# Kernel optimization log

Hardware: AMD Instinct MI355X
Metric: run time of the kernel (lower is better)

Reference implementation:

```python
import jax, jax.numpy as jnp
import numpy as np
import math

B, T, F, H, A = 32, 2048, 2048, 1024, 512


def setup_inputs() -> dict:
    key = jax.random.key(0)
    ks = jax.random.split(key, 8)
    def xavier(k, shape):
        fan_out, fan_in = shape
        bound = math.sqrt(6.0 / (fan_in + fan_out))
        return jax.random.uniform(k, shape, jnp.float32, -bound, bound)
    return {
        "features": jax.random.normal(ks[0], (B, T, F), jnp.float32),
        "hidden": jax.random.normal(ks[1], (B, H), jnp.float32),
        "W_h": xavier(ks[2], (A, H)),
        "b_h": jnp.zeros((A,), jnp.float32),
        "W_a": xavier(ks[3], (A, F)),
        "b_a": jnp.zeros((A,), jnp.float32),
        "v_w": xavier(ks[4], (1, A)),
        "v_b": jnp.zeros((1,), jnp.float32),
    }


def reference(features, hidden, W_h, b_h, W_a, b_a, v_w, v_b):
    # h_proj: [B, 1, A]; a_proj: [B, T, A]
    h_proj = (hidden @ W_h.T + b_h)[:, None, :]
    a_proj = jnp.einsum('btf,af->bta', features, W_a) + b_a
    # energy: [B, T]
    energy = (jnp.tanh(h_proj + a_proj) @ v_w[0] + v_b[0]) / math.sqrt(W_h.shape[0])
    alpha = jax.nn.softmax(energy, axis=1)
    context = jnp.einsum('bt,btf->bf', alpha, features)
    return (context, alpha)
```

## Files before the change

kernel.cpp:

```cpp
#include <hip/hip_runtime.h>
#include <hip/hip_bf16.h>
#include <math.h>

#define B_ 32
#define T_ 2048
#define F_ 2048
#define H_ 1024
#define A_ 512

typedef __attribute__((ext_vector_type(8))) short short8;
typedef __attribute__((ext_vector_type(4))) float f32x4;

__device__ __forceinline__ unsigned short f2bf(float x) {
  union { float f; unsigned int u; } v; v.f = x;
  unsigned int r = v.u + 0x7FFFu + ((v.u >> 16) & 1u);
  return (unsigned short)(r >> 16);
}

#define GLOAD_LDS16(gp, lp) __builtin_amdgcn_global_load_lds( \
    (const __attribute__((address_space(1))) void*)(gp), \
    (__attribute__((address_space(3))) void*)(lp), 16, 0, 0)

#define SBAR   asm volatile("s_barrier" ::: "memory")
#define WAITV0 asm volatile("s_waitcnt vmcnt(0)" ::: "memory")
#define WAITL0 asm volatile("s_waitcnt lgkmcnt(0)" ::: "memory")
#define SCHEDB __builtin_amdgcn_sched_barrier(0)

__global__ __launch_bounds__(256) void k_convert_wa(const float* __restrict__ wa,
                                                    unsigned short* __restrict__ out) {
  int i = (blockIdx.x * 256 + threadIdx.x) * 4;
  float4 v = *(const float4*)(wa + i);
  ushort4 o;
  o.x = f2bf(v.x); o.y = f2bf(v.y); o.z = f2bf(v.z); o.w = f2bf(v.w);
  *(ushort4*)(out + i) = o;
}

__global__ __launch_bounds__(256) void k_hproj(const float* __restrict__ hidden,
                                               const float* __restrict__ Wh,
                                               const float* __restrict__ bh,
                                               const float* __restrict__ ba,
                                               float* __restrict__ hcomb) {
  int gw = (blockIdx.x * 256 + threadIdx.x) >> 6;
  int lane = threadIdx.x & 63;
  int b = gw >> 9, a = gw & 511;
  const float* wr = Wh + a * H_;
  const float* hr = hidden + b * H_;
  float acc = 0.f;
  #pragma unroll
  for (int k = 0; k < H_; k += 256) {
    float4 wv = *(const float4*)(wr + k + lane * 4);
    float4 hv = *(const float4*)(hr + k + lane * 4);
    acc += wv.x * hv.x + wv.y * hv.y + wv.z * hv.z + wv.w * hv.w;
  }
  #pragma unroll
  for (int off = 32; off; off >>= 1) acc += __shfl_xor(acc, off);
  if (lane == 0) hcomb[gw] = acc + bh[a] + ba[a];
}

__global__ __launch_bounds__(512, 4) void k_energy(
    const float* __restrict__ feat, const unsigned short* __restrict__ wab,
    const float* __restrict__ hcomb, const float* __restrict__ vw,
    const float* __restrict__ vb, float* __restrict__ energy) {
  __shared__ __align__(16) char smem[78848];

  const int tid = threadIdx.x;
  const int lane = tid & 63;
  const int w = tid >> 6;
  const int wm = w >> 2, wn = w & 3;
  const int lrow = lane & 15, lk = lane >> 4;
  const int m0 = blockIdx.x * 64;
  const int bb = m0 >> 11;

  float* s_h = (float*)(smem + 73728);
  float* s_v = (float*)(smem + 75776);

  const unsigned short* bsrc0 = wab + (size_t)(tid >> 2) * 2048 +
      ((((tid & 3) - ((tid >> 3) & 3)) & 3) << 3);
  const float* asrc = feat + (size_t)(m0 + (tid >> 3)) * 2048 + ((tid & 7) << 2);
  const int aw_off = ((tid >> 3) << 6) +
      ((((((tid >> 1) & 3) + ((tid >> 4) & 3)) & 3)) << 4) + ((tid & 1) << 3);

  const int psl = ((lk + (lrow >> 1)) & 3) << 4;
  const int a_roff = ((wm * 32 + lrow) << 6) + psl;
  const int b_roff = ((wn * 128 + lrow) << 6) + psl;

  f32x4 acc[2][8] = {};

  s_h[tid] = hcomb[bb * 512 + tid];
  s_v[tid] = vw[tid];
  {
    char* bd = smem + (w << 10);
    GLOAD_LDS16(bsrc0,              bd);
    GLOAD_LDS16(bsrc0 + 128 * 2048, bd + 8192);
    GLOAD_LDS16(bsrc0 + 256 * 2048, bd + 16384);
    GLOAD_LDS16(bsrc0 + 384 * 2048, bd + 24576);
    float4 av = *(const float4*)(asrc);
    WAITV0; SCHEDB;
    ushort4 ap;
    ap.x = f2bf(av.x); ap.y = f2bf(av.y); ap.z = f2bf(av.z); ap.w = f2bf(av.w);
    *(ushort4*)(smem + 65536 + aw_off) = ap;
    WAITL0; SBAR;
  }

  #pragma unroll 2
  for (int t = 0; t < 64; ++t) {
    const int cur = t & 1, nxt = cur ^ 1;
    const int k1 = ((t + 1) & 63) << 5;
    const unsigned short* bs = bsrc0 + k1;
    char* bd = smem + nxt * 32768 + (w << 10);
    GLOAD_LDS16(bs,              bd);
    GLOAD_LDS16(bs + 128 * 2048, bd + 8192);
    GLOAD_LDS16(bs + 256 * 2048, bd + 16384);
    GLOAD_LDS16(bs + 384 * 2048, bd + 24576);
    float4 av = *(const float4*)(asrc + k1);

    const char* Ab = smem + 65536 + cur * 4096 + a_roff;
    const char* Bb = smem + cur * 32768 + b_roff;
    short8 a0 = *(const short8*)(Ab);
    short8 a1 = *(const short8*)(Ab + 1024);
    short8 b0 = *(const short8*)(Bb);
    short8 b1 = *(const short8*)(Bb + 1024);
    short8 b2 = *(const short8*)(Bb + 2048);
    short8 b3 = *(const short8*)(Bb + 3072);
    acc[0][0] = __builtin_amdgcn_mfma_f32_16x16x32_bf16(a0, b0, acc[0][0], 0, 0, 0);
    acc[1][0] = __builtin_amdgcn_mfma_f32_16x16x32_bf16(a1, b0, acc[1][0], 0, 0, 0);
    acc[0][1] = __builtin_amdgcn_mfma_f32_16x16x32_bf16(a0, b1, acc[0][1], 0, 0, 0);
    acc[1][1] = __builtin_amdgcn_mfma_f32_16x16x32_bf16(a1, b1, acc[1][1], 0, 0, 0);
    acc[0][2] = __builtin_amdgcn_mfma_f32_16x16x32_bf16(a0, b2, acc[0][2], 0, 0, 0);
    acc[1][2] = __builtin_amdgcn_mfma_f32_16x16x32_bf16(a1, b2, acc[1][2], 0, 0, 0);
    acc[0][3] = __builtin_amdgcn_mfma_f32_16x16x32_bf16(a0, b3, acc[0][3], 0, 0, 0);
    acc[1][3] = __builtin_amdgcn_mfma_f32_16x16x32_bf16(a1, b3, acc[1][3], 0, 0, 0);
    short8 b4 = *(const short8*)(Bb + 4096);
    short8 b5 = *(const short8*)(Bb + 5120);
    short8 b6 = *(const short8*)(Bb + 6144);
    short8 b7 = *(const short8*)(Bb + 7168);
    acc[0][4] = __builtin_amdgcn_mfma_f32_16x16x32_bf16(a0, b4, acc[0][4], 0, 0, 0);
    acc[1][4] = __builtin_amdgcn_mfma_f32_16x16x32_bf16(a1, b4, acc[1][4], 0, 0, 0);
    acc[0][5] = __builtin_amdgcn_mfma_f32_16x16x32_bf16(a0, b5, acc[0][5], 0, 0, 0);
    acc[1][5] = __builtin_amdgcn_mfma_f32_16x16x32_bf16(a1, b5, acc[1][5], 0, 0, 0);
    acc[0][6] = __builtin_amdgcn_mfma_f32_16x16x32_bf16(a0, b6, acc[0][6], 0, 0, 0);
    acc[1][6] = __builtin_amdgcn_mfma_f32_16x16x32_bf16(a1, b6, acc[1][6], 0, 0, 0);
    acc[0][7] = __builtin_amdgcn_mfma_f32_16x16x32_bf16(a0, b7, acc[0][7], 0, 0, 0);
    acc[1][7] = __builtin_amdgcn_mfma_f32_16x16x32_bf16(a1, b7, acc[1][7], 0, 0, 0);

    ushort4 ap;
    ap.x = f2bf(av.x); ap.y = f2bf(av.y); ap.z = f2bf(av.z); ap.w = f2bf(av.w);
    *(ushort4*)(smem + 65536 + nxt * 4096 + aw_off) = ap;

    WAITL0;
    WAITV0;
    SBAR;
  }

  float (*e_red)[4] = (float(*)[4])(smem + 77824);
  const float vbv = vb[0];
  #pragma unroll
  for (int mi = 0; mi < 2; ++mi) {
    #pragma unroll
    for (int j = 0; j < 4; ++j) {
      float s = 0.f;
      #pragma unroll
      for (int ni = 0; ni < 8; ++ni) {
        int col = wn * 128 + ni * 16 + lrow;
        float x = acc[mi][ni][j] + s_h[col];
        s += tanhf(x) * s_v[col];
      }
      s += __shfl_xor(s, 1); s += __shfl_xor(s, 2);
      s += __shfl_xor(s, 4); s += __shfl_xor(s, 8);
      if (lrow == 0) e_red[wm * 32 + mi * 16 + (lane >> 4) * 4 + j][wn] = s;
    }
  }
  __syncthreads();
  if (tid < 64) {
    float s = e_red[tid][0] + e_red[tid][1] + e_red[tid][2] + e_red[tid][3];
    energy[m0 + tid] = (s + vbv) * 0.04419417382415922f;
  }
}

__global__ __launch_bounds__(256) void k_softmax(const float* __restrict__ energy,
                                                 float* __restrict__ alpha) {
  const int b = blockIdx.x, tid = threadIdx.x;
  const float* e = energy + b * T_;
  float4 v0 = ((const float4*)e)[tid * 2];
  float4 v1 = ((const float4*)e)[tid * 2 + 1];
  float m = fmaxf(fmaxf(fmaxf(v0.x, v0.y), fmaxf(v0.z, v0.w)),
                  fmaxf(fmaxf(v1.x, v1.y), fmaxf(v1.z, v1.w)));
  #pragma unroll
  for (int off = 32; off; off >>= 1) m = fmaxf(m, __shfl_xor(m, off));
  __shared__ float rmax[4], rsum[4];
  const int lane = tid & 63, wv = tid >> 6;
  if (!lane) rmax[wv] = m;
  __syncthreads();
  m = fmaxf(fmaxf(rmax[0], rmax[1]), fmaxf(rmax[2], rmax[3]));
  float x0 = expf(v0.x - m), x1 = expf(v0.y - m), x2 = expf(v0.z - m), x3 = expf(v0.w - m);
  float x4 = expf(v1.x - m), x5 = expf(v1.y - m), x6 = expf(v1.z - m), x7 = expf(v1.w - m);
  float s = ((x0 + x1) + (x2 + x3)) + ((x4 + x5) + (x6 + x7));
  #pragma unroll
  for (int off = 32; off; off >>= 1) s += __shfl_xor(s, off);
  if (!lane) rsum[wv] = s;
  __syncthreads();
  s = (rsum[0] + rsum[1]) + (rsum[2] + rsum[3]);
  float inv = 1.f / s;
  float4 o0 = {x0 * inv, x1 * inv, x2 * inv, x3 * inv};
  float4 o1 = {x4 * inv, x5 * inv, x6 * inv, x7 * inv};
  float* ao = alpha + b * T_;
  ((float4*)ao)[tid * 2] = o0;
  ((float4*)ao)[tid * 2 + 1] = o1;
}

__global__ __launch_bounds__(256) void k_ctx_partial(const float* __restrict__ feat,
                                                     const float* __restrict__ alpha,
                                                     float* __restrict__ part) {
  const int b = blockIdx.x, fh = blockIdx.y, tc = blockIdx.z;
  const int tid = threadIdx.x;
  __shared__ float sa[128];
  if (tid < 128) sa[tid] = alpha[b * T_ + tc * 128 + tid];
  __syncthreads();
  const int f = fh * 1024 + tid * 4;
  const float* fp = feat + ((size_t)(b * T_ + tc * 128)) * F_ + f;
  float4 s = {0.f, 0.f, 0.f, 0.f};
  #pragma unroll 4
  for (int t = 0; t < 128; ++t) {
    float a = sa[t];
    float4 v = *(const float4*)(fp + (size_t)t * F_);
    s.x += a * v.x; s.y += a * v.y; s.z += a * v.z; s.w += a * v.w;
  }
  *(float4*)(part + ((size_t)(b * 16 + tc)) * F_ + f) = s;
}

__global__ __launch_bounds__(256) void k_ctx_reduce(const float* __restrict__ part,
                                                    float* __restrict__ ctx) {
  const int i4 = blockIdx.x * 256 + threadIdx.x;
  const int b = i4 >> 9, f4 = i4 & 511;
  const float4* p = (const float4*)part;
  float4 s = {0.f, 0.f, 0.f, 0.f};
  #pragma unroll
  for (int tc = 0; tc < 16; ++tc) {
    float4 v = p[((b * 16 + tc) << 9) + f4];
    s.x += v.x; s.y += v.y; s.z += v.z; s.w += v.w;
  }
  ((float4*)ctx)[i4] = s;
}

extern "C" void kernel_launch(void* const* d_in, const int* in_sizes, int n_in,
                              void* d_out, int out_size, void* d_ws, size_t ws_size,
                              hipStream_t stream) {
  const float* feat   = (const float*)d_in[0];
  const float* hidden = (const float*)d_in[1];
  const float* Wh     = (const float*)d_in[2];
  const float* bh     = (const float*)d_in[3];
  const float* Wa     = (const float*)d_in[4];
  const float* ba     = (const float*)d_in[5];
  const float* vw     = (const float*)d_in[6];
  const float* vb     = (const float*)d_in[7];

  float* ctx   = (float*)d_out;
  float* alpha = (float*)d_out + B_ * T_;

  char* ws = (char*)d_ws;
  unsigned short* wab = (unsigned short*)ws;
  float* hcomb  = (float*)(ws + 2097152);
  float* energy = (float*)(ws + 2097152 + 65536);
  float* part   = (float*)(ws + 2097152 + 65536 + 262144);

  k_convert_wa<<<dim3(1024), dim3(256), 0, stream>>>(Wa, wab);
  k_hproj<<<dim3(4096), dim3(256), 0, stream>>>(hidden, Wh, bh, ba, hcomb);
  k_energy<<<dim3(1024), dim3(512), 0, stream>>>(feat, wab, hcomb, vw, vb, energy);
  k_softmax<<<dim3(32), dim3(256), 0, stream>>>(energy, alpha);
  k_ctx_partial<<<dim3(32, 2, 16), dim3(256), 0, stream>>>(feat, alpha, part);
  k_ctx_reduce<<<dim3(64), dim3(256), 0, stream>>>(part, ctx);
}
```

Baseline: 354.6 us.

## Prefetch fp32 feature tile two steps ahead with partial vmcnt wait

The fp32 feature loads for the A operand are now issued two K-steps ahead into alternating registers (avA/avB), so each iteration waits with vmcnt(1) instead of draining every outstanding global load. This is meant to hide global-load latency of the A tile behind a full iteration of MFMA work. The loop is manually unrolled by two with sched barriers to pin the ordering. The cost is extra registers, and correctness relies on the in-order vmcnt accounting between the LDS-direct loads and the register load.

```diff
diff --git a/kernel.cpp b/kernel.cpp
--- a/kernel.cpp
+++ b/kernel.cpp
@@ -22,9 +22,8 @@
     (__attribute__((address_space(3))) void*)(lp), 16, 0, 0)
 
 #define SBAR   asm volatile("s_barrier" ::: "memory")
-#define WAITV0 asm volatile("s_waitcnt vmcnt(0)" ::: "memory")
-#define WAITL0 asm volatile("s_waitcnt lgkmcnt(0)" ::: "memory")
 #define SCHEDB __builtin_amdgcn_sched_barrier(0)
+#define WAIT_V1_L0 asm volatile("s_waitcnt vmcnt(1) lgkmcnt(0)" ::: "memory")
 
 __global__ __launch_bounds__(256) void k_convert_wa(const float* __restrict__ wa,
                                                     unsigned short* __restrict__ out) {
@@ -85,72 +84,85 @@
   const int b_roff = ((wn * 128 + lrow) << 6) + psl;
 
   f32x4 acc[2][8] = {};
+  float4 avA, avB;
 
   s_h[tid] = hcomb[bb * 512 + tid];
   s_v[tid] = vw[tid];
   {
+    avA = *(const float4*)(asrc);
     char* bd = smem + (w << 10);
     GLOAD_LDS16(bsrc0,              bd);
     GLOAD_LDS16(bsrc0 + 128 * 2048, bd + 8192);
     GLOAD_LDS16(bsrc0 + 256 * 2048, bd + 16384);
     GLOAD_LDS16(bsrc0 + 384 * 2048, bd + 24576);
-    float4 av = *(const float4*)(asrc);
-    WAITV0; SCHEDB;
+    SCHEDB;
+    avB = *(const float4*)(asrc + 32);
+    SCHEDB;
     ushort4 ap;
-    ap.x = f2bf(av.x); ap.y = f2bf(av.y); ap.z = f2bf(av.z); ap.w = f2bf(av.w);
+    ap.x = f2bf(avA.x); ap.y = f2bf(avA.y); ap.z = f2bf(avA.z); ap.w = f2bf(avA.w);
     *(ushort4*)(smem + 65536 + aw_off) = ap;
-    WAITL0; SBAR;
-  }
-
-  #pragma unroll 2
-  for (int t = 0; t < 64; ++t) {
-    const int cur = t & 1, nxt = cur ^ 1;
-    const int k1 = ((t + 1) & 63) << 5;
-    const unsigned short* bs = bsrc0 + k1;
-    char* bd = smem + nxt * 32768 + (w << 10);
-    GLOAD_LDS16(bs,              bd);
-    GLOAD_LDS16(bs + 128 * 2048, bd + 8192);
-    GLOAD_LDS16(bs + 256 * 2048, bd + 16384);
-    GLOAD_LDS16(bs + 384 * 2048, bd + 24576);
-    float4 av = *(const float4*)(asrc + k1);
-
-    const char* Ab = smem + 65536 + cur * 4096 + a_roff;
-    const char* Bb = smem + cur * 32768 + b_roff;
-    short8 a0 = *(const short8*)(Ab);
-    short8 a1 = *(const short8*)(Ab + 1024);
-    short8 b0 = *(const short8*)(Bb);
-    short8 b1 = *(const short8*)(Bb + 1024);
-    short8 b2 = *(const short8*)(Bb + 2048);
-    short8 b3 = *(const short8*)(Bb + 3072);
-    acc[0][0] = __builtin_amdgcn_mfma_f32_16x16x32_bf16(a0, b0, acc[0][0], 0, 0, 0);
-    acc[1][0] = __builtin_amdgcn_mfma_f32_16x16x32_bf16(a1, b0, acc[1][0], 0, 0, 0);
-    acc[0][1] = __builtin_amdgcn_mfma_f32_16x16x32_bf16(a0, b1, acc[0][1], 0, 0, 0);
-    acc[1][1] = __builtin_amdgcn_mfma_f32_16x16x32_bf16(a1, b1, acc[1][1], 0, 0, 0);
-    acc[0][2] = __builtin_amdgcn_mfma_f32_16x16x32_bf16(a0, b2, acc[0][2], 0, 0, 0);
-    acc[1][2] = __builtin_amdgcn_mfma_f32_16x16x32_bf16(a1, b2, acc[1][2], 0, 0, 0);
-    acc[0][3] = __builtin_amdgcn_mfma_f32_16x16x32_bf16(a0, b3, acc[0][3], 0, 0, 0);
-    acc[1][3] = __builtin_amdgcn_mfma_f32_16x16x32_bf16(a1, b3, acc[1][3], 0, 0, 0);
-    short8 b4 = *(const short8*)(Bb + 4096);
-    short8 b5 = *(const short8*)(Bb + 5120);
-    short8 b6 = *(const short8*)(Bb + 6144);
-    short8 b7 = *(const short8*)(Bb + 7168);
-    acc[0][4] = __builtin_amdgcn_mfma_f32_16x16x32_bf16(a0, b4, acc[0][4], 0, 0, 0);
-    acc[1][4] = __builtin_amdgcn_mfma_f32_16x16x32_bf16(a1, b4, acc[1][4], 0, 0, 0);
-    acc[0][5] = __builtin_amdgcn_mfma_f32_16x16x32_bf16(a0, b5, acc[0][5], 0, 0, 0);
-    acc[1][5] = __builtin_amdgcn_mfma_f32_16x16x32_bf16(a1, b5, acc[1][5], 0, 0, 0);
-    acc[0][6] = __builtin_amdgcn_mfma_f32_16x16x32_bf16(a0, b6, acc[0][6], 0, 0, 0);
-    acc[1][6] = __builtin_amdgcn_mfma_f32_16x16x32_bf16(a1, b6, acc[1][6], 0, 0, 0);
-    acc[0][7] = __builtin_amdgcn_mfma_f32_16x16x32_bf16(a0, b7, acc[0][7], 0, 0, 0);
-    acc[1][7] = __builtin_amdgcn_mfma_f32_16x16x32_bf16(a1, b7, acc[1][7], 0, 0, 0);
-
-    ushort4 ap;
-    ap.x = f2bf(av.x); ap.y = f2bf(av.y); ap.z = f2bf(av.z); ap.w = f2bf(av.w);
-    *(ushort4*)(smem + 65536 + nxt * 4096 + aw_off) = ap;
-
-    WAITL0;
-    WAITV0;
+    SCHEDB;
+    WAIT_V1_L0;
     SBAR;
   }
+
+#define ENERGY_BODY(CUR, NXT, CONS, SLOT, K1, K2) do {                        \
+    const unsigned short* bs_ = bsrc0 + (K1);                                 \
+    char* bd_ = smem + (NXT) * 32768 + (w << 10);                             \
+    GLOAD_LDS16(bs_,              bd_);                                       \
+    GLOAD_LDS16(bs_ + 128 * 2048, bd_ + 8192);                                \
+    GLOAD_LDS16(bs_ + 256 * 2048, bd_ + 16384);                               \
+    GLOAD_LDS16(bs_ + 384 * 2048, bd_ + 24576);                               \
+    SCHEDB;                                                                   \
+    {                                                                         \
+      const char* Ab = smem + 65536 + (CUR) * 4096 + a_roff;                  \
+      const char* Bb = smem + (CUR) * 32768 + b_roff;                         \
+      short8 a0 = *(const short8*)(Ab);                                       \
+      short8 a1 = *(const short8*)(Ab + 1024);                                \
+      short8 b0 = *(const short8*)(Bb);                                       \
+      short8 b1 = *(const short8*)(Bb + 1024);                                \
+      short8 b2 = *(const short8*)(Bb + 2048);                                \
+      short8 b3 = *(const short8*)(Bb + 3072);                                \
+      acc[0][0] = __builtin_amdgcn_mfma_f32_16x16x32_bf16(a0, b0, acc[0][0], 0, 0, 0); \
+      acc[1][0] = __builtin_amdgcn_mfma_f32_16x16x32_bf16(a1, b0, acc[1][0], 0, 0, 0); \
+      acc[0][1] = __builtin_amdgcn_mfma_f32_16x16x32_bf16(a0, b1, acc[0][1], 0, 0, 0); \
+      acc[1][1] = __builtin_amdgcn_mfma_f32_16x16x32_bf16(a1, b1, acc[1][1], 0, 0, 0); \
+      acc[0][2] = __builtin_amdgcn_mfma_f32_16x16x32_bf16(a0, b2, acc[0][2], 0, 0, 0); \
+      acc[1][2] = __builtin_amdgcn_mfma_f32_16x16x32_bf16(a1, b2, acc[1][2], 0, 0, 0); \
+      acc[0][3] = __builtin_amdgcn_mfma_f32_16x16x32_bf16(a0, b3, acc[0][3], 0, 0, 0); \
+      acc[1][3] = __builtin_amdgcn_mfma_f32_16x16x32_bf16(a1, b3, acc[1][3], 0, 0, 0); \
+      short8 b4 = *(const short8*)(Bb + 4096);                                \
+      short8 b5 = *(const short8*)(Bb + 5120);                                \
+      short8 b6 = *(const short8*)(Bb + 6144);                                \
+      short8 b7 = *(const short8*)(Bb + 7168);                                \
+      acc[0][4] = __builtin_amdgcn_mfma_f32_16x16x32_bf16(a0, b4, acc[0][4], 0, 0, 0); \
+      acc[1][4] = __builtin_amdgcn_mfma_f32_16x16x32_bf16(a1, b4, acc[1][4], 0, 0, 0); \
+      acc[0][5] = __builtin_amdgcn_mfma_f32_16x16x32_bf16(a0, b5, acc[0][5], 0, 0, 0); \
+      acc[1][5] = __builtin_amdgcn_mfma_f32_16x16x32_bf16(a1, b5, acc[1][5], 0, 0, 0); \
+      acc[0][6] = __builtin_amdgcn_mfma_f32_16x16x32_bf16(a0, b6, acc[0][6], 0, 0, 0); \
+      acc[1][6] = __builtin_amdgcn_mfma_f32_16x16x32_bf16(a1, b6, acc[1][6], 0, 0, 0); \
+      acc[0][7] = __builtin_amdgcn_mfma_f32_16x16x32_bf16(a0, b7, acc[0][7], 0, 0, 0); \
+      acc[1][7] = __builtin_amdgcn_mfma_f32_16x16x32_bf16(a1, b7, acc[1][7], 0, 0, 0); \
+    }                                                                         \
+    {                                                                         \
+      ushort4 ap_;       \
+      ap_.x = f2bf((CONS).x); ap_.y = f2bf((CONS).y);                         \
+      ap_.z = f2bf((CONS).z); ap_.w = f2bf((CONS).w);                         \
+      *(ushort4*)(smem + 65536 + (NXT) * 4096 + aw_off) = ap_;                \
+    }                                                                         \
+    SCHEDB;                                                                   \
+    (SLOT) = *(const float4*)(asrc + (K2));               \
+    SCHEDB;                                                                   \
+    WAIT_V1_L0;    \
+    SBAR;                                                                     \
+  } while (0)
+
+  #pragma unroll 1
+  for (int t = 0; t < 64; t += 2) {
+    ENERGY_BODY(0, 1, avB, avA, (((t + 1) & 63) << 5), (((t + 2) & 63) << 5));
+    ENERGY_BODY(1, 0, avA, avB, (((t + 2) & 63) << 5), (((t + 3) & 63) << 5));
+  }
+#undef ENERGY_BODY
 
   float (*e_red)[4] = (float(*)[4])(smem + 77824);
   const float vbv = vb[0];
```

After: 343.9 us. 1.03x faster.
